# Performance work log

Measured on AMD Instinct MI355X. Metric: run time of the kernel, lower is better.

## Reference

```python
import jax, jax.numpy as jnp
import numpy as np

N, E, NIN, NOUT, H = 50000, 800000, 128, 128, 8
C = NOUT // H  # head dim = 16


def setup_inputs() -> dict:
    key = jax.random.key(0)
    ks = jax.random.split(key, 12)
    s = 1.0 / np.sqrt(NIN)
    return {
        "x": jax.random.normal(ks[0], (N, NIN), dtype=jnp.float32),
        "edge_index": jax.random.randint(ks[1], (2, E), 0, N),
        "edge_attr": jax.random.normal(ks[2], (E, NIN), dtype=jnp.float32),
        "Wq": jax.random.normal(ks[3], (NIN, H * C), dtype=jnp.float32) * s,
        "bq": jnp.zeros((H * C,), dtype=jnp.float32),
        "Wk": jax.random.normal(ks[4], (NIN, H * C), dtype=jnp.float32) * s,
        "bk": jnp.zeros((H * C,), dtype=jnp.float32),
        "Wv": jax.random.normal(ks[5], (NIN, H * C), dtype=jnp.float32) * s,
        "bv": jnp.zeros((H * C,), dtype=jnp.float32),
        "We": jax.random.normal(ks[6], (NIN, H * C), dtype=jnp.float32) * s,  # lin_edge, bias=False in PyG
        "Wskip": jax.random.normal(ks[7], (NIN, H * C), dtype=jnp.float32) * s,
        "bskip": jnp.zeros((H * C,), dtype=jnp.float32),
    }


def reference(x, edge_index, edge_attr, Wq, bq, Wk, bk, Wv, bv, We, Wskip, bskip):
    src = edge_index[0]  # j (source / message sender)
    dst = edge_index[1]  # i (destination / aggregation target)

    q = (x @ Wq + bq).reshape(N, H, C)
    k = (x @ Wk + bk).reshape(N, H, C)
    v = (x @ Wv + bv).reshape(N, H, C)
    e = (edge_attr @ We).reshape(E, H, C)

    k_e = k[src] + e                                   # [E,H,C]
    alpha = jnp.einsum('ehc,ehc->eh', q[dst], k_e) / jnp.sqrt(jnp.float32(C))

    # segment softmax over incoming edges of each destination node
    m = jax.ops.segment_max(alpha, dst, num_segments=N)            # [N,H]
    a = jnp.exp(alpha - m[dst])                                    # [E,H]
    z = jax.ops.segment_sum(a, dst, num_segments=N)                # [N,H]
    a = a / (z[dst] + 1e-16)

    msg = (v[src] + e) * a[:, :, None]                             # [E,H,C]
    out = jax.ops.segment_sum(msg, dst, num_segments=N)            # [N,H,C]
    out = out.reshape(N, H * C) + (x @ Wskip + bskip)              # root skip
    return out
```

## Files before the change

kernel.cpp:

```cpp
#include <hip/hip_runtime.h>


#define N_NODES 50000
#define N_EDGES 800000
#define DIN     128
#define DHC     128
#define NHEAD   8
#define HDIM    16
#define LDK     72
#define LDAT    132

static_assert(N_EDGES % 128 == 0, "edge tiles exact");

typedef short bf16x8 __attribute__((ext_vector_type(8)));
typedef float f32x4  __attribute__((ext_vector_type(4)));

#define MFMA(a, b, c) __builtin_amdgcn_mfma_f32_16x16x32_bf16((a), (b), (c), 0, 0, 0)

__device__ __forceinline__ void split4(const float4 v, uint2& hi, uint2& lo) {
    uint a0 = __float_as_uint(v.x), a1 = __float_as_uint(v.y);
    uint a2 = __float_as_uint(v.z), a3 = __float_as_uint(v.w);
    hi.x = (a1 & 0xFFFF0000u) | (a0 >> 16);
    hi.y = (a3 & 0xFFFF0000u) | (a2 >> 16);
    float d0 = v.x - __uint_as_float(a0 & 0xFFFF0000u);
    float d1 = v.y - __uint_as_float(a1 & 0xFFFF0000u);
    float d2 = v.z - __uint_as_float(a2 & 0xFFFF0000u);
    float d3 = v.w - __uint_as_float(a3 & 0xFFFF0000u);
    uint b0 = __float_as_uint(d0), b1 = __float_as_uint(d1);
    uint b2 = __float_as_uint(d2), b3 = __float_as_uint(d3);
    lo.x = (b1 & 0xFFFF0000u) | (b0 >> 16);
    lo.y = (b3 & 0xFFFF0000u) | (b2 >> 16);
}

__global__ __launch_bounds__(256) void prep_weights(
    const float* __restrict__ Wq, const float* __restrict__ Wk,
    const float* __restrict__ Wv, const float* __restrict__ Wskip,
    const float* __restrict__ We,
    ushort* __restrict__ WTh, ushort* __restrict__ WTl)
{
    const float* W;
    switch (blockIdx.y) {
        case 0: W = Wq; break;  case 1: W = Wk; break;
        case 2: W = Wv; break;  case 3: W = Wskip; break;
        default: W = We; break;
    }
    ushort* th = WTh + (size_t)blockIdx.y * DIN * DHC;
    ushort* tl = WTl + (size_t)blockIdx.y * DIN * DHC;

    for (int i = blockIdx.x * 256 + threadIdx.x; i < DIN * 32; i += 1024) {
        int k  = i >> 5;
        int c4 = (i & 31) * 4;
        float4 v = ((const float4*)(W + (size_t)k * DHC))[i & 31];
        float e[4] = {v.x, v.y, v.z, v.w};
        #pragma unroll
        for (int j = 0; j < 4; ++j) {
            uint a = __float_as_uint(e[j]);
            th[(c4 + j) * DIN + k] = (ushort)(a >> 16);
            float d = e[j] - __uint_as_float(a & 0xFFFF0000u);
            tl[(c4 + j) * DIN + k] = (ushort)(__float_as_uint(d) >> 16);
        }
    }
}

__global__ __launch_bounds__(256) void node_gemm_mfma(
    const float* __restrict__ x,
    const ushort* __restrict__ WTh, const ushort* __restrict__ WTl,
    const float* __restrict__ bq, const float* __restrict__ bk,
    const float* __restrict__ bv, const float* __restrict__ bskip,
    float* __restrict__ Q, float* __restrict__ K,
    float* __restrict__ V, float* __restrict__ SKIP)
{
    __shared__ ushort sAh[128 * LDK], sAl[128 * LDK];
    __shared__ ushort sBh[128 * LDK], sBl[128 * LDK];

    const int m = blockIdx.y;
    const float* bias; float* OUT;
    switch (m) {
        case 0:  bias = bq;    OUT = Q;    break;
        case 1:  bias = bk;    OUT = K;    break;
        case 2:  bias = bv;    OUT = V;    break;
        default: bias = bskip; OUT = SKIP; break;
    }
    const ushort* wh = WTh + (size_t)m * DIN * DHC;
    const ushort* wl = WTl + (size_t)m * DIN * DHC;

    const int tid  = threadIdx.x;
    const int row0 = blockIdx.x * 128;
    const int lane = tid & 63;
    const int wv   = tid >> 6;
    const int lr   = lane & 15;
    const int lk   = lane >> 4;

    f32x4 acc[8][2];
    #pragma unroll
    for (int i = 0; i < 8; ++i) { acc[i][0] = (f32x4)0.f; acc[i][1] = (f32x4)0.f; }

    for (int kk = 0; kk < DIN; kk += 64) {
        #pragma unroll
        for (int p = 0; p < 4; ++p) {
            int i = tid + p * 256;
            int c = i >> 3, g = i & 7;
            *(uint4*)&sBh[c * LDK + 8 * g] = *(const uint4*)(wh + c * DIN + kk + 8 * g);
            *(uint4*)&sBl[c * LDK + 8 * g] = *(const uint4*)(wl + c * DIN + kk + 8 * g);
        }
        #pragma unroll
        for (int p = 0; p < 8; ++p) {
            int row = (tid >> 4) + 16 * p;
            int c4  = tid & 15;
            int r   = row0 + row;
            float4 v = (r < N_NODES)
                ? ((const float4*)(x + (size_t)r * DIN + kk))[c4]
                : make_float4(0.f, 0.f, 0.f, 0.f);
            uint2 h, l; split4(v, h, l);
            *(uint2*)&sAh[row * LDK + 4 * c4] = h;
            *(uint2*)&sAl[row * LDK + 4 * c4] = l;
        }
        __syncthreads();

        #pragma unroll
        for (int ks = 0; ks < 2; ++ks) {
            const int kb = ks * 32 + lk * 8;
            bf16x8 bh0 = *(const bf16x8*)&sBh[(wv * 32 +      lr) * LDK + kb];
            bf16x8 bh1 = *(const bf16x8*)&sBh[(wv * 32 + 16 + lr) * LDK + kb];
            bf16x8 bl0 = *(const bf16x8*)&sBl[(wv * 32 +      lr) * LDK + kb];
            bf16x8 bl1 = *(const bf16x8*)&sBl[(wv * 32 + 16 + lr) * LDK + kb];
            #pragma unroll
            for (int rf = 0; rf < 8; ++rf) {
                bf16x8 ah = *(const bf16x8*)&sAh[(rf * 16 + lr) * LDK + kb];
                bf16x8 al = *(const bf16x8*)&sAl[(rf * 16 + lr) * LDK + kb];
                acc[rf][0] = MFMA(ah, bh0, acc[rf][0]);
                acc[rf][0] = MFMA(al, bh0, acc[rf][0]);
                acc[rf][0] = MFMA(ah, bl0, acc[rf][0]);
                acc[rf][1] = MFMA(ah, bh1, acc[rf][1]);
                acc[rf][1] = MFMA(al, bh1, acc[rf][1]);
                acc[rf][1] = MFMA(ah, bl1, acc[rf][1]);
            }
        }
        __syncthreads();
    }

    const float b0 = bias[wv * 32 + lr];
    const float b1 = bias[wv * 32 + 16 + lr];
    #pragma unroll
    for (int rf = 0; rf < 8; ++rf) {
        #pragma unroll
        for (int reg = 0; reg < 4; ++reg) {
            int r = row0 + rf * 16 + lk * 4 + reg;
            if (r < N_NODES) {
                OUT[(size_t)r * DHC + wv * 32 +      lr] = acc[rf][0][reg] + b0;
                OUT[(size_t)r * DHC + wv * 32 + 16 + lr] = acc[rf][1][reg] + b1;
            }
        }
    }
}

__global__ __launch_bounds__(256) void hist_kernel(
    const int* __restrict__ eidx, int* __restrict__ cnt)
{
    for (int i = blockIdx.x * 256 + threadIdx.x; i < N_EDGES; i += gridDim.x * 256)
        atomicAdd(&cnt[eidx[N_EDGES + i]], 1);
}

__global__ __launch_bounds__(1024) void scan_kernel(
    const int* __restrict__ cnt, int* __restrict__ cursor)
{
    __shared__ int buf[2][1024];
    const int tid = threadIdx.x;
    const int chunk = (N_NODES + 1023) / 1024;
    const int base = tid * chunk;
    int s = 0;
    for (int i = 0; i < chunk; ++i) {
        int idx = base + i;
        if (idx < N_NODES) s += cnt[idx];
    }
    buf[0][tid] = s;
    __syncthreads();
    int cur = 0;
    for (int off = 1; off < 1024; off <<= 1) {
        int v = buf[cur][tid];
        if (tid >= off) v += buf[cur][tid - off];
        buf[cur ^ 1][tid] = v;
        __syncthreads();
        cur ^= 1;
    }
    int run = buf[cur][tid] - s;
    for (int i = 0; i < chunk; ++i) {
        int idx = base + i;
        if (idx < N_NODES) {
            cursor[idx] = run;
            run += cnt[idx];
        }
    }
}

__global__ __launch_bounds__(256) void scatter_kernel(
    const int* __restrict__ eidx, int* __restrict__ cursor,
    int4* __restrict__ s_meta)
{
    for (int i = blockIdx.x * 256 + threadIdx.x; i < N_EDGES; i += gridDim.x * 256) {
        int sv = eidx[i];
        int d  = eidx[N_EDGES + i];
        int pos = atomicAdd(&cursor[d], 1);
        s_meta[pos] = make_int4(sv, d, i, 0);
    }
}

__global__ __launch_bounds__(256) void edge_kernel(
    const float* __restrict__ edge_attr,
    const ushort* __restrict__ WTh, const ushort* __restrict__ WTl,
    const int4* __restrict__ s_meta,
    const float* __restrict__ Qf, const float* __restrict__ Kf,
    const float* __restrict__ Vf,
    float* __restrict__ OUT,
    float* __restrict__ Z)
{
    __shared__ __align__(16) char poolraw[4 * 128 * LDK * 2];
    __shared__ float sw[128 * NHEAD];
    __shared__ int   sSrc[128], sDst[128], sEid[128];
    __shared__ unsigned long long smask[2];
    __shared__ int   runstart[130];

    ushort* sAh = (ushort*)poolraw;
    ushort* sAl = sAh + 128 * LDK;
    ushort* sBh = sAl + 128 * LDK;
    ushort* sBl = sBh + 128 * LDK;
    float*  ep  = (float*)poolraw;

    const ushort* wh = WTh + 4 * DIN * DHC;
    const ushort* wl = WTl + 4 * DIN * DHC;

    const int tid  = threadIdx.x;
    const int lane = tid & 63;
    const int wv   = tid >> 6;
    const int lr   = lane & 15;
    const int lk   = lane >> 4;
    const int nTiles = N_EDGES / 128;

    for (int tile = blockIdx.x; tile < nTiles; tile += gridDim.x) {
        const int e0 = tile * 128;
        __syncthreads();

        if (tid < 128) {
            int4 mm = s_meta[e0 + tid];
            sSrc[tid] = mm.x; sDst[tid] = mm.y; sEid[tid] = mm.z;
        }
        __syncthreads();

        f32x4 acc[8][2];
        #pragma unroll
        for (int i = 0; i < 8; ++i) { acc[i][0] = (f32x4)0.f; acc[i][1] = (f32x4)0.f; }

        for (int kk = 0; kk < DIN; kk += 64) {
            #pragma unroll
            for (int p = 0; p < 4; ++p) {
                int i = tid + p * 256;
                int c = i >> 3, g = i & 7;
                *(uint4*)&sBh[c * LDK + 8 * g] = *(const uint4*)(wh + c * DIN + kk + 8 * g);
                *(uint4*)&sBl[c * LDK + 8 * g] = *(const uint4*)(wl + c * DIN + kk + 8 * g);
            }
            #pragma unroll
            for (int p = 0; p < 8; ++p) {
                int row = (tid >> 4) + 16 * p;
                int c4  = tid & 15;
                float4 v = ((const float4*)(edge_attr + (size_t)sEid[row] * DIN + kk))[c4];
                uint2 h, l; split4(v, h, l);
                *(uint2*)&sAh[row * LDK + 4 * c4] = h;
                *(uint2*)&sAl[row * LDK + 4 * c4] = l;
            }
            __syncthreads();

            #pragma unroll
            for (int ks = 0; ks < 2; ++ks) {
                const int kb = ks * 32 + lk * 8;
                bf16x8 bh0 = *(const bf16x8*)&sBh[(wv * 32 +      lr) * LDK + kb];
                bf16x8 bh1 = *(const bf16x8*)&sBh[(wv * 32 + 16 + lr) * LDK + kb];
                bf16x8 bl0 = *(const bf16x8*)&sBl[(wv * 32 +      lr) * LDK + kb];
                bf16x8 bl1 = *(const bf16x8*)&sBl[(wv * 32 + 16 + lr) * LDK + kb];
                #pragma unroll
                for (int rf = 0; rf < 8; ++rf) {
                    bf16x8 ah = *(const bf16x8*)&sAh[(rf * 16 + lr) * LDK + kb];
                    bf16x8 al = *(const bf16x8*)&sAl[(rf * 16 + lr) * LDK + kb];
                    acc[rf][0] = MFMA(ah, bh0, acc[rf][0]);
                    acc[rf][0] = MFMA(al, bh0, acc[rf][0]);
                    acc[rf][0] = MFMA(ah, bl0, acc[rf][0]);
                    acc[rf][1] = MFMA(ah, bh1, acc[rf][1]);
                    acc[rf][1] = MFMA(al, bh1, acc[rf][1]);
                    acc[rf][1] = MFMA(ah, bl1, acc[rf][1]);
                }
            }
            __syncthreads();
        }

        #pragma unroll
        for (int rf = 0; rf < 8; ++rf) {
            #pragma unroll
            for (int reg = 0; reg < 4; ++reg) {
                int row = rf * 16 + lk * 4 + reg;
                ep[row * LDAT + wv * 32 +      lr] = acc[rf][0][reg];
                ep[row * LDAT + wv * 32 + 16 + lr] = acc[rf][1][reg];
            }
        }
        __syncthreads();

        #pragma unroll
        for (int t = 0; t < 4; ++t) {
            int task = tid + t * 256;
            int el   = task & 127;
            int h    = task >> 7;
            int src  = sSrc[el];
            int dst  = sDst[el];
            const float4* qp = (const float4*)(Qf + (size_t)dst * DHC + h * HDIM);
            const float4* kp = (const float4*)(Kf + (size_t)src * DHC + h * HDIM);
            const float4* vp = (const float4*)(Vf + (size_t)src * DHC + h * HDIM);
            float4* epp = (float4*)&ep[el * LDAT + h * HDIM];

            float4 e4[4], q4[4], k4[4];
            #pragma unroll
            for (int r = 0; r < 4; ++r) { e4[r] = epp[r]; q4[r] = qp[r]; k4[r] = kp[r]; }

            float alpha = 0.f;
            #pragma unroll
            for (int r = 0; r < 4; ++r) {
                alpha = fmaf(q4[r].x, k4[r].x + e4[r].x, alpha);
                alpha = fmaf(q4[r].y, k4[r].y + e4[r].y, alpha);
                alpha = fmaf(q4[r].z, k4[r].z + e4[r].z, alpha);
                alpha = fmaf(q4[r].w, k4[r].w + e4[r].w, alpha);
            }
            float w = __expf(alpha * 0.25f);
            sw[el * NHEAD + h] = w;
            #pragma unroll
            for (int r = 0; r < 4; ++r) {
                float4 v4 = vp[r];
                epp[r] = make_float4(w * (v4.x + e4[r].x), w * (v4.y + e4[r].y),
                                     w * (v4.z + e4[r].z), w * (v4.w + e4[r].w));
            }
        }

        if (tid < 128) {
            bool flag = (tid == 0) || (sDst[tid] != sDst[tid - 1]);
            unsigned long long m = __ballot(flag);
            if ((tid & 63) == 0) smask[tid >> 6] = m;
        }
        __syncthreads();

        const unsigned long long m0 = smask[0], m1 = smask[1];
        const int nruns = __popcll(m0) + __popcll(m1);
        if (tid < 128) {
            bool flag = (tid == 0) || (sDst[tid] != sDst[tid - 1]);
            if (flag) {
                int rid;
                if (tid < 64) rid = __popcll(m0 & ((1ull << tid) - 1));
                else          rid = __popcll(m0) + __popcll(m1 & ((1ull << (tid - 64)) - 1));
                runstart[rid] = tid;
            }
        }
        if (tid == 0) runstart[nruns] = 128;
        __syncthreads();

        for (int t = tid; t < nruns * NHEAD; t += 256) {
            int r = t >> 3, h = t & 7;
            int s0 = runstart[r], s1 = runstart[r + 1];
            float s = 0.f;
            for (int el = s0; el < s1; ++el) s += sw[el * NHEAD + h];
            int dst = sDst[s0];
            if (r == 0 || r == nruns - 1) atomicAdd(&Z[(size_t)dst * NHEAD + h], s);
            else                          Z[(size_t)dst * NHEAD + h] = s;
        }

        for (int t = tid; t < nruns * 32; t += 256) {
            int r = t >> 5, c = t & 31;
            int s0 = runstart[r], s1 = runstart[r + 1];
            float4 s = make_float4(0.f, 0.f, 0.f, 0.f);
            for (int el = s0; el < s1; ++el) {
                float4 v = *(const float4*)&ep[el * LDAT + c * 4];
                s.x += v.x; s.y += v.y; s.z += v.z; s.w += v.w;
            }
            int dst = sDst[s0];
            float* ob = OUT + (size_t)dst * DHC + c * 4;
            if (r == 0 || r == nruns - 1) {
                atomicAdd(ob + 0, s.x); atomicAdd(ob + 1, s.y);
                atomicAdd(ob + 2, s.z); atomicAdd(ob + 3, s.w);
            } else {
                *(float4*)ob = s;
            }
        }
    }
}

__global__ __launch_bounds__(256) void finalize_kernel(
    float* __restrict__ OUT, const float* __restrict__ Z,
    const float* __restrict__ SKIP)
{
    size_t idx = (size_t)blockIdx.x * 256 + threadIdx.x;
    if (idx >= (size_t)N_NODES * DHC) return;
    int n = (int)(idx >> 7);
    int h = ((int)idx & 127) >> 4;
    OUT[idx] = OUT[idx] / (Z[(size_t)n * NHEAD + h] + 1e-16f) + SKIP[idx];
}

extern "C" void kernel_launch(void* const* d_in, const int* in_sizes, int n_in,
                              void* d_out, int out_size, void* d_ws, size_t ws_size,
                              hipStream_t stream)
{
    const float* x         = (const float*)d_in[0];
    const int*   eidx      = (const int*)  d_in[1];
    const float* edge_attr = (const float*)d_in[2];
    const float* Wq    = (const float*)d_in[3];
    const float* bq    = (const float*)d_in[4];
    const float* Wk    = (const float*)d_in[5];
    const float* bk    = (const float*)d_in[6];
    const float* Wv    = (const float*)d_in[7];
    const float* bv    = (const float*)d_in[8];
    const float* We    = (const float*)d_in[9];
    const float* Wskip = (const float*)d_in[10];
    const float* bskip = (const float*)d_in[11];
    float* out = (float*)d_out;

    char* wsb = (char*)d_ws;
    const size_t npf = (size_t)N_NODES * DHC;
    float* Q      = (float*)wsb;                          wsb += npf * 4;
    float* K      = (float*)wsb;                          wsb += npf * 4;
    float* V      = (float*)wsb;                          wsb += npf * 4;
    float* SKIP   = (float*)wsb;                          wsb += npf * 4;
    float* Z      = (float*)wsb;                          wsb += (size_t)N_NODES * NHEAD * 4;
    int*   cnt    = (int*)wsb;                            wsb += (size_t)N_NODES * 4;
    int*   cursor = (int*)wsb;                            wsb += (size_t)N_NODES * 4;
    int4*  s_meta = (int4*)wsb;                           wsb += (size_t)N_EDGES * 16;
    ushort* WTh   = (ushort*)wsb;                         wsb += (size_t)5 * DIN * DHC * 2;
    ushort* WTl   = (ushort*)wsb;

    hipMemsetAsync(out, 0, npf * sizeof(float), stream);
    hipMemsetAsync(Z, 0, (size_t)N_NODES * NHEAD * sizeof(float), stream);
    hipMemsetAsync(cnt, 0, (size_t)N_NODES * sizeof(int), stream);

    prep_weights<<<dim3(4, 5), 256, 0, stream>>>(Wq, Wk, Wv, Wskip, We, WTh, WTl);

    node_gemm_mfma<<<dim3((N_NODES + 127) / 128, 4), 256, 0, stream>>>(
        x, WTh, WTl, bq, bk, bv, bskip, Q, K, V, SKIP);

    hist_kernel<<<1024, 256, 0, stream>>>(eidx, cnt);
    scan_kernel<<<1, 1024, 0, stream>>>(cnt, cursor);
    scatter_kernel<<<1024, 256, 0, stream>>>(eidx, cursor, s_meta);

    edge_kernel<<<1024, 256, 0, stream>>>(edge_attr, WTh, WTl, s_meta,
                                          Q, K, V, out, Z);

    finalize_kernel<<<(int)((npf + 255) / 256), 256, 0, stream>>>(out, Z, SKIP);
}
```

Baseline: 1.101 ms.

## Halve edge tile, read weights from global, prefetch second K-half

The edge kernel now processes 64-edge tiles instead of 128, which shrinks shared memory. The node and edge GEMMs drop the shared-memory staging of the split-bf16 weights and load weight fragments straight from global/L2 into registers. The second 64-column half of the A operand is prefetched into registers while the first half is being multiplied. The aim is higher occupancy and less LDS traffic and fewer barriers, at the cost of more global weight reads per tile. It also clamps the exp argument.

```diff
diff --git a/kernel.cpp b/kernel.cpp
--- a/kernel.cpp
+++ b/kernel.cpp
@@ -9,8 +9,9 @@
 #define HDIM    16
 #define LDK     72
 #define LDAT    132
-
-static_assert(N_EDGES % 128 == 0, "edge tiles exact");
+#define ETILE   64
+
+static_assert(N_EDGES % ETILE == 0, "edge tiles exact");
 
 typedef short bf16x8 __attribute__((ext_vector_type(8)));
 typedef float f32x4  __attribute__((ext_vector_type(4)));
@@ -71,7 +72,6 @@
     float* __restrict__ V, float* __restrict__ SKIP)
 {
     __shared__ ushort sAh[128 * LDK], sAl[128 * LDK];
-    __shared__ ushort sBh[128 * LDK], sBl[128 * LDK];
 
     const int m = blockIdx.y;
     const float* bias; float* OUT;
@@ -95,35 +95,40 @@
     #pragma unroll
     for (int i = 0; i < 8; ++i) { acc[i][0] = (f32x4)0.f; acc[i][1] = (f32x4)0.f; }
 
+    #pragma unroll
+    for (int p = 0; p < 8; ++p) {
+        int row = (tid >> 4) + 16 * p;
+        int c4  = tid & 15;
+        int r   = row0 + row;
+        float4 v = (r < N_NODES) ? ((const float4*)(x + (size_t)r * DIN))[c4]
+                                 : make_float4(0.f, 0.f, 0.f, 0.f);
+        uint2 h, l; split4(v, h, l);
+        *(uint2*)&sAh[row * LDK + 4 * c4] = h;
+        *(uint2*)&sAl[row * LDK + 4 * c4] = l;
+    }
+    __syncthreads();
+
+    float4 pf[8];
+    #pragma unroll
+    for (int p = 0; p < 8; ++p) {
+        int row = (tid >> 4) + 16 * p;
+        int c4  = tid & 15;
+        int r   = row0 + row;
+        pf[p] = (r < N_NODES) ? ((const float4*)(x + (size_t)r * DIN + 64))[c4]
+                              : make_float4(0.f, 0.f, 0.f, 0.f);
+    }
+
+    #pragma unroll
     for (int kk = 0; kk < DIN; kk += 64) {
-        #pragma unroll
-        for (int p = 0; p < 4; ++p) {
-            int i = tid + p * 256;
-            int c = i >> 3, g = i & 7;
-            *(uint4*)&sBh[c * LDK + 8 * g] = *(const uint4*)(wh + c * DIN + kk + 8 * g);
-            *(uint4*)&sBl[c * LDK + 8 * g] = *(const uint4*)(wl + c * DIN + kk + 8 * g);
-        }
-        #pragma unroll
-        for (int p = 0; p < 8; ++p) {
-            int row = (tid >> 4) + 16 * p;
-            int c4  = tid & 15;
-            int r   = row0 + row;
-            float4 v = (r < N_NODES)
-                ? ((const float4*)(x + (size_t)r * DIN + kk))[c4]
-                : make_float4(0.f, 0.f, 0.f, 0.f);
-            uint2 h, l; split4(v, h, l);
-            *(uint2*)&sAh[row * LDK + 4 * c4] = h;
-            *(uint2*)&sAl[row * LDK + 4 * c4] = l;
-        }
-        __syncthreads();
-
         #pragma unroll
         for (int ks = 0; ks < 2; ++ks) {
             const int kb = ks * 32 + lk * 8;
-            bf16x8 bh0 = *(const bf16x8*)&sBh[(wv * 32 +      lr) * LDK + kb];
-            bf16x8 bh1 = *(const bf16x8*)&sBh[(wv * 32 + 16 + lr) * LDK + kb];
-            bf16x8 bl0 = *(const bf16x8*)&sBl[(wv * 32 +      lr) * LDK + kb];
-            bf16x8 bl1 = *(const bf16x8*)&sBl[(wv * 32 + 16 + lr) * LDK + kb];
+            const size_t boff0 = (size_t)(wv * 32 +      lr) * DIN + kk + kb;
+            const size_t boff1 = (size_t)(wv * 32 + 16 + lr) * DIN + kk + kb;
+            bf16x8 bh0 = *(const bf16x8*)(wh + boff0);
+            bf16x8 bh1 = *(const bf16x8*)(wh + boff1);
+            bf16x8 bl0 = *(const bf16x8*)(wl + boff0);
+            bf16x8 bl1 = *(const bf16x8*)(wl + boff1);
             #pragma unroll
             for (int rf = 0; rf < 8; ++rf) {
                 bf16x8 ah = *(const bf16x8*)&sAh[(rf * 16 + lr) * LDK + kb];
@@ -137,6 +142,17 @@
             }
         }
         __syncthreads();
+        if (kk == 0) {
+            #pragma unroll
+            for (int p = 0; p < 8; ++p) {
+                int row = (tid >> 4) + 16 * p;
+                int c4  = tid & 15;
+                uint2 h, l; split4(pf[p], h, l);
+                *(uint2*)&sAh[row * LDK + 4 * c4] = h;
+                *(uint2*)&sAl[row * LDK + 4 * c4] = l;
+            }
+            __syncthreads();
+        }
     }
 
     const float b0 = bias[wv * 32 + lr];
@@ -214,17 +230,15 @@
     float* __restrict__ OUT,
     float* __restrict__ Z)
 {
-    __shared__ __align__(16) char poolraw[4 * 128 * LDK * 2];
-    __shared__ float sw[128 * NHEAD];
-    __shared__ int   sSrc[128], sDst[128], sEid[128];
-    __shared__ unsigned long long smask[2];
-    __shared__ int   runstart[130];
-
-    ushort* sAh = (ushort*)poolraw;
-    ushort* sAl = sAh + 128 * LDK;
-    ushort* sBh = sAl + 128 * LDK;
-    ushort* sBl = sBh + 128 * LDK;
-    float*  ep  = (float*)poolraw;
+    __shared__ __align__(16) float pool[ETILE * LDAT];
+    __shared__ float sw[ETILE * NHEAD];
+    __shared__ int   sSrc[ETILE], sDst[ETILE], sEid[ETILE];
+    __shared__ unsigned long long smask;
+    __shared__ int   runstart[ETILE + 2];
+
+    ushort* sAh = (ushort*)pool;
+    ushort* sAl = sAh + ETILE * LDK;
+    float*  ep  = pool;
 
     const ushort* wh = WTh + 4 * DIN * DHC;
     const ushort* wl = WTl + 4 * DIN * DHC;
@@ -234,50 +248,54 @@
     const int wv   = tid >> 6;
     const int lr   = lane & 15;
     const int lk   = lane >> 4;
-    const int nTiles = N_EDGES / 128;
+    const int nTiles = N_EDGES / ETILE;
 
     for (int tile = blockIdx.x; tile < nTiles; tile += gridDim.x) {
-        const int e0 = tile * 128;
-        __syncthreads();
-
-        if (tid < 128) {
+        const int e0 = tile * ETILE;
+        __syncthreads();
+
+        if (tid < ETILE) {
             int4 mm = s_meta[e0 + tid];
             sSrc[tid] = mm.x; sDst[tid] = mm.y; sEid[tid] = mm.z;
         }
         __syncthreads();
 
-        f32x4 acc[8][2];
-        #pragma unroll
-        for (int i = 0; i < 8; ++i) { acc[i][0] = (f32x4)0.f; acc[i][1] = (f32x4)0.f; }
-
+        #pragma unroll
+        for (int p = 0; p < 4; ++p) {
+            int row = (tid >> 4) + 16 * p;
+            int c4  = tid & 15;
+            float4 v = ((const float4*)(edge_attr + (size_t)sEid[row] * DIN))[c4];
+            uint2 h, l; split4(v, h, l);
+            *(uint2*)&sAh[row * LDK + 4 * c4] = h;
+            *(uint2*)&sAl[row * LDK + 4 * c4] = l;
+        }
+        __syncthreads();
+
+        float4 pf[4];
+        #pragma unroll
+        for (int p = 0; p < 4; ++p) {
+            int row = (tid >> 4) + 16 * p;
+            int c4  = tid & 15;
+            pf[p] = ((const float4*)(edge_attr + (size_t)sEid[row] * DIN + 64))[c4];
+        }
+
+        f32x4 acc[4][2];
+        #pragma unroll
+        for (int i = 0; i < 4; ++i) { acc[i][0] = (f32x4)0.f; acc[i][1] = (f32x4)0.f; }
+
+        #pragma unroll
         for (int kk = 0; kk < DIN; kk += 64) {
-            #pragma unroll
-            for (int p = 0; p < 4; ++p) {
-                int i = tid + p * 256;
-                int c = i >> 3, g = i & 7;
-                *(uint4*)&sBh[c * LDK + 8 * g] = *(const uint4*)(wh + c * DIN + kk + 8 * g);
-                *(uint4*)&sBl[c * LDK + 8 * g] = *(const uint4*)(wl + c * DIN + kk + 8 * g);
-            }
-            #pragma unroll
-            for (int p = 0; p < 8; ++p) {
-                int row = (tid >> 4) + 16 * p;
-                int c4  = tid & 15;
-                float4 v = ((const float4*)(edge_attr + (size_t)sEid[row] * DIN + kk))[c4];
-                uint2 h, l; split4(v, h, l);
-                *(uint2*)&sAh[row * LDK + 4 * c4] = h;
-                *(uint2*)&sAl[row * LDK + 4 * c4] = l;
-            }
-            __syncthreads();
-
             #pragma unroll
             for (int ks = 0; ks < 2; ++ks) {
                 const int kb = ks * 32 + lk * 8;
-                bf16x8 bh0 = *(const bf16x8*)&sBh[(wv * 32 +      lr) * LDK + kb];
-                bf16x8 bh1 = *(const bf16x8*)&sBh[(wv * 32 + 16 + lr) * LDK + kb];
-                bf16x8 bl0 = *(const bf16x8*)&sBl[(wv * 32 +      lr) * LDK + kb];
-                bf16x8 bl1 = *(const bf16x8*)&sBl[(wv * 32 + 16 + lr) * LDK + kb];
+                const size_t boff0 = (size_t)(wv * 32 +      lr) * DIN + kk + kb;
+                const size_t boff1 = (size_t)(wv * 32 + 16 + lr) * DIN + kk + kb;
+                bf16x8 bh0 = *(const bf16x8*)(wh + boff0);
+                bf16x8 bh1 = *(const bf16x8*)(wh + boff1);
+                bf16x8 bl0 = *(const bf16x8*)(wl + boff0);
+                bf16x8 bl1 = *(const bf16x8*)(wl + boff1);
                 #pragma unroll
-                for (int rf = 0; rf < 8; ++rf) {
+                for (int rf = 0; rf < 4; ++rf) {
                     bf16x8 ah = *(const bf16x8*)&sAh[(rf * 16 + lr) * LDK + kb];
                     bf16x8 al = *(const bf16x8*)&sAl[(rf * 16 + lr) * LDK + kb];
                     acc[rf][0] = MFMA(ah, bh0, acc[rf][0]);
@@ -289,10 +307,21 @@
                 }
             }
             __syncthreads();
-        }
-
-        #pragma unroll
-        for (int rf = 0; rf < 8; ++rf) {
+            if (kk == 0) {
+                #pragma unroll
+                for (int p = 0; p < 4; ++p) {
+                    int row = (tid >> 4) + 16 * p;
+                    int c4  = tid & 15;
+                    uint2 h, l; split4(pf[p], h, l);
+                    *(uint2*)&sAh[row * LDK + 4 * c4] = h;
+                    *(uint2*)&sAl[row * LDK + 4 * c4] = l;
+                }
+                __syncthreads();
+            }
+        }
+
+        #pragma unroll
+        for (int rf = 0; rf < 4; ++rf) {
             #pragma unroll
             for (int reg = 0; reg < 4; ++reg) {
                 int row = rf * 16 + lk * 4 + reg;
@@ -303,10 +332,10 @@
         __syncthreads();
 
         #pragma unroll
-        for (int t = 0; t < 4; ++t) {
+        for (int t = 0; t < 2; ++t) {
             int task = tid + t * 256;
-            int el   = task & 127;
-            int h    = task >> 7;
+            int el   = task & 63;
+            int h    = task >> 6;
             int src  = sSrc[el];
             int dst  = sDst[el];
             const float4* qp = (const float4*)(Qf + (size_t)dst * DHC + h * HDIM);
@@ -326,7 +355,7 @@
                 alpha = fmaf(q4[r].z, k4[r].z + e4[r].z, alpha);
                 alpha = fmaf(q4[r].w, k4[r].w + e4[r].w, alpha);
             }
-            float w = __expf(alpha * 0.25f);
+            float w = __expf(fminf(alpha * 0.25f, 30.f));
             sw[el * NHEAD + h] = w;
             #pragma unroll
             for (int r = 0; r < 4; ++r) {
@@ -336,25 +365,23 @@
             }
         }
 
-        if (tid < 128) {
+        if (tid < 64) {
             bool flag = (tid == 0) || (sDst[tid] != sDst[tid - 1]);
             unsigned long long m = __ballot(flag);
-            if ((tid & 63) == 0) smask[tid >> 6] = m;
-        }
-        __syncthreads();
-
-        const unsigned long long m0 = smask[0], m1 = smask[1];
-        const int nruns = __popcll(m0) + __popcll(m1);
-        if (tid < 128) {
+            if (tid == 0) smask = m;
+        }
+        __syncthreads();
+
+        const unsigned long long m0 = smask;
+        const int nruns = __popcll(m0);
+        if (tid < 64) {
             bool flag = (tid == 0) || (sDst[tid] != sDst[tid - 1]);
             if (flag) {
-                int rid;
-                if (tid < 64) rid = __popcll(m0 & ((1ull << tid) - 1));
-                else          rid = __popcll(m0) + __popcll(m1 & ((1ull << (tid - 64)) - 1));
+                int rid = __popcll(m0 & ((1ull << tid) - 1));
                 runstart[rid] = tid;
             }
         }
-        if (tid == 0) runstart[nruns] = 128;
+        if (tid == 0) runstart[nruns] = ETILE;
         __syncthreads();
 
         for (int t = tid; t < nruns * NHEAD; t += 256) {
```

Result: no change. 1.082 ms (-1.7%).
